# Kernel optimization log

Hardware: AMD Instinct MI355X
Metric: run time of the kernel (lower is better)

The kernel has to match this reference:

```python
import jax, jax.numpy as jnp
import numpy as np

B, L, H, V = 16, 512, 256, 32000
HALF = H // 2
EPS_LN = 1e-5
EPS_NORM = 1e-12


def setup_inputs() -> dict:
    key = jax.random.key(0)
    ks = jax.random.split(key, 9)
    s = 0.02
    return {
        "seq": jax.random.randint(ks[0], (B, L), 0, V),
        "embed": jax.random.normal(ks[1], (V, H), jnp.float32) * s,
        "W1": jax.random.normal(ks[2], (2 * H, H), jnp.float32) * s,
        "b1": jnp.zeros((2 * H,), jnp.float32),
        "W2": jax.random.normal(ks[3], (H, 2 * H), jnp.float32) * s,
        "b2": jnp.zeros((H,), jnp.float32),
        "gamma": jnp.ones((H,), jnp.float32),
        "beta": jnp.zeros((H,), jnp.float32),
        "W_sem": jax.random.normal(ks[4], (HALF, H), jnp.float32) * s,
        "W_epi": jax.random.normal(ks[5], (HALF, H), jnp.float32) * s,
        "W_rp": jax.random.normal(ks[6], (H, H), jnp.float32) * s,
        "b_rp": jnp.zeros((H,), jnp.float32),
        "W_out": jax.random.normal(ks[7], (V, H), jnp.float32) * s,
        "b_out": jnp.zeros((V,), jnp.float32),
    }


def _l2norm(x):
    # F.normalize(dim=-1): x / max(||x||, eps)
    n = jnp.sqrt(jnp.sum(x * x, axis=-1, keepdims=True))
    return x / jnp.maximum(n, EPS_NORM)


def reference(seq, embed, W1, b1, W2, b2, gamma, beta, W_sem, W_epi, W_rp, b_rp, W_out, b_out):
    h = embed[seq]                                   # [B, L, H]
    ff = jnp.maximum(h @ W1.T + b1, 0.0) @ W2.T + b2  # MLP with 2H hidden
    x = h + ff
    mu = jnp.mean(x, axis=-1, keepdims=True)
    var = jnp.var(x, axis=-1, keepdims=True)
    h = (x - mu) / jnp.sqrt(var + EPS_LN) * gamma + beta  # LayerNorm

    ks_all = jnp.einsum('blh,kh->blk', h, W_sem)     # [B, L, HALF]
    ke_all = jnp.einsum('blh,kh->blk', h, W_epi)

    def step(carry, kv):
        M_s, M_e = carry
        k_s, k_e = kv                                 # [B, HALF] each
        kns = _l2norm(k_s)
        kne = _l2norm(k_e)
        vps = jnp.einsum('bij,bj->bi', M_s, kns)      # read from fast weights
        vpe = jnp.einsum('bij,bj->bi', M_e, kne)
        M_s = M_s + jnp.einsum('bi,bj->bij', k_s - vps, kns)  # delta-rule write
        M_e = M_e + jnp.einsum('bi,bj->bij', k_e - vpe, kne)
        return (M_s, M_e), None

    M0 = jnp.zeros((B, HALF, HALF), h.dtype)
    # scan over timesteps 0..L-2 (time-major)
    (M_s, M_e), _ = jax.lax.scan(
        step, (M0, M0),
        (jnp.swapaxes(ks_all[:, :-1], 0, 1), jnp.swapaxes(ke_all[:, :-1], 0, 1)))

    cs = jnp.einsum('bij,bj->bi', M_s, ks_all[:, -1])  # read with last-token query
    ce = jnp.einsum('bij,bj->bi', M_e, ke_all[:, -1])
    c = jnp.concatenate([cs, ce], axis=-1)             # [B, H]
    r = c @ W_rp.T + b_rp
    return r @ W_out.T + b_out                          # [B, V]
```

## Files before the change

kernel.cpp:

```cpp
#include <hip/hip_runtime.h>

#define B_ 16
#define L_ 512
#define H_ 256
#define V_ 32000
#define HALF_ 128

typedef __attribute__((ext_vector_type(8))) short short8;
typedef __attribute__((ext_vector_type(4))) float floatx4;

__device__ __forceinline__ unsigned short f2bf(float x) {
  unsigned int u = __float_as_uint(x);
  unsigned int r = (u + 0x7FFFu + ((u >> 16) & 1u)) >> 16;
  return (unsigned short)r;
}

template <int CTRL>
__device__ __forceinline__ float dpp_xor_add(float x) {
  int y = __builtin_amdgcn_mov_dpp(__float_as_int(x), CTRL, 0xf, 0xf, true);
  return x + __int_as_float(y);
}

__device__ __forceinline__ float redu16(float p) {
  p = dpp_xor_add<0xB1>(p);
  p = dpp_xor_add<0x4E>(p);
  p = dpp_xor_add<0x141>(p);
  p = dpp_xor_add<0x140>(p);
  return p;
}

__device__ __forceinline__ void async_cp16(const float* g, float* l) {
  __builtin_amdgcn_global_load_lds(
      (const __attribute__((address_space(1))) void*)g,
      (__attribute__((address_space(3))) void*)l, 16, 0, 0);
}

__global__ __launch_bounds__(256) void prep_kernel(const int* __restrict__ seq,
                                                   const float* __restrict__ embed,
                                                   float* __restrict__ h,
                                                   unsigned short* __restrict__ hbf,
                                                   const float* __restrict__ W1,
                                                   const float* __restrict__ W2,
                                                   const float* __restrict__ Ws,
                                                   const float* __restrict__ We,
                                                   unsigned short* __restrict__ W1b,
                                                   unsigned short* __restrict__ W2b,
                                                   unsigned short* __restrict__ Wcb) {
  int blk = blockIdx.x;
  int tid = threadIdx.x;
  if (blk < 2048) {
    int token = blk * 4 + (tid >> 6);
    int lane = tid & 63;
    int row = seq[token];
    float4 v = ((const float4*)(embed + (size_t)row * H_))[lane];
    ((float4*)(h + (size_t)token * H_))[lane] = v;
    ushort4 o;
    o.x = f2bf(v.x); o.y = f2bf(v.y); o.z = f2bf(v.z); o.w = f2bf(v.w);
    *(ushort4*)(hbf + (size_t)token * H_ + lane * 4) = o;
  } else {
    int i = (blk - 2048) * 256 + tid;
    if (i < 131072) W1b[i] = f2bf(W1[i]);
    else if (i < 262144) W2b[i - 131072] = f2bf(W2[i - 131072]);
    else if (i < 294912) Wcb[i - 262144] = f2bf(Ws[i - 262144]);
    else Wcb[i - 262144] = f2bf(We[i - 294912]);
  }
}

template <int MT, bool RELU, bool BIAS, bool RES, bool OUT_BF16>
__global__ __launch_bounds__(256) void gemm_mfma(const unsigned short* __restrict__ A,
                                                 const unsigned short* __restrict__ Bw,
                                                 const float* __restrict__ bias,
                                                 const float* __restrict__ Res,
                                                 float* __restrict__ Cf,
                                                 unsigned short* __restrict__ Cb,
                                                 int M, int N, int K) {
  constexpr int FI = MT / 32;
  __shared__ unsigned short As[MT * 40];
  __shared__ unsigned short Bs[128 * 40];
  int tid = threadIdx.x;
  int wave = tid >> 6, lane = tid & 63;
  int wm = (wave >> 1) * (MT / 2), wn = (wave & 1) * 64;
  int quad = lane >> 4, l15 = lane & 15;
  int bm = blockIdx.y * MT, bn = blockIdx.x * 128;
  int sr = tid >> 2, sq = tid & 3;

  floatx4 zero = {0.f, 0.f, 0.f, 0.f};
  floatx4 acc[FI][4];
#pragma unroll
  for (int fi = 0; fi < FI; fi++)
#pragma unroll
    for (int fj = 0; fj < 4; fj++) acc[fi][fj] = zero;

  uint4 av0, av1, bv0, bv1;
  av0 = *(const uint4*)(A + (size_t)(bm + sr) * K + sq * 8);
  if (MT == 128) av1 = *(const uint4*)(A + (size_t)(bm + 64 + sr) * K + sq * 8);
  bv0 = *(const uint4*)(Bw + (size_t)(bn + sr) * K + sq * 8);
  bv1 = *(const uint4*)(Bw + (size_t)(bn + 64 + sr) * K + sq * 8);

  for (int k0 = 0; k0 < K; k0 += 32) {
    __syncthreads();
    *(uint4*)(As + sr * 40 + sq * 8) = av0;
    if (MT == 128) *(uint4*)(As + (64 + sr) * 40 + sq * 8) = av1;
    *(uint4*)(Bs + sr * 40 + sq * 8) = bv0;
    *(uint4*)(Bs + (64 + sr) * 40 + sq * 8) = bv1;
    __syncthreads();
    if (k0 + 32 < K) {
      av0 = *(const uint4*)(A + (size_t)(bm + sr) * K + k0 + 32 + sq * 8);
      if (MT == 128) av1 = *(const uint4*)(A + (size_t)(bm + 64 + sr) * K + k0 + 32 + sq * 8);
      bv0 = *(const uint4*)(Bw + (size_t)(bn + sr) * K + k0 + 32 + sq * 8);
      bv1 = *(const uint4*)(Bw + (size_t)(bn + 64 + sr) * K + k0 + 32 + sq * 8);
    }
    short8 af[FI], bf[4];
#pragma unroll
    for (int f = 0; f < FI; f++) af[f] = *(const short8*)(As + (wm + f * 16 + l15) * 40 + quad * 8);
#pragma unroll
    for (int f = 0; f < 4; f++) bf[f] = *(const short8*)(Bs + (wn + f * 16 + l15) * 40 + quad * 8);
#pragma unroll
    for (int fi = 0; fi < FI; fi++)
#pragma unroll
      for (int fj = 0; fj < 4; fj++)
        acc[fi][fj] = __builtin_amdgcn_mfma_f32_16x16x32_bf16(af[fi], bf[fj], acc[fi][fj], 0, 0, 0);
  }

#pragma unroll
  for (int fi = 0; fi < FI; fi++) {
#pragma unroll
    for (int fj = 0; fj < 4; fj++) {
      int col = bn + wn + fj * 16 + l15;
      float bb = BIAS ? bias[col] : 0.f;
#pragma unroll
      for (int rg = 0; rg < 4; rg++) {
        int row = bm + wm + fi * 16 + quad * 4 + rg;
        float v = acc[fi][fj][rg] + bb;
        if (RES) v += Res[(size_t)row * N + col];
        if (RELU) v = fmaxf(v, 0.f);
        if (OUT_BF16) Cb[(size_t)row * N + col] = f2bf(v);
        else Cf[(size_t)row * N + col] = v;
      }
    }
  }
}

__global__ void ln_kernel(const float* __restrict__ x, const float* __restrict__ gamma,
                          const float* __restrict__ beta, unsigned short* __restrict__ yb) {
  int row = blockIdx.x;
  int lane = threadIdx.x;
  float4 v = ((const float4*)(x + (size_t)row * H_))[lane];
  float s = v.x + v.y + v.z + v.w;
  float sq = v.x * v.x + v.y * v.y + v.z * v.z + v.w * v.w;
#pragma unroll
  for (int off = 32; off >= 1; off >>= 1) {
    s += __shfl_xor(s, off);
    sq += __shfl_xor(sq, off);
  }
  float mu = s * (1.f / H_);
  float var = sq * (1.f / H_) - mu * mu;
  float inv = rsqrtf(var + 1e-5f);
  float4 g = ((const float4*)gamma)[lane];
  float4 b = ((const float4*)beta)[lane];
  ushort4 o;
  o.x = f2bf((v.x - mu) * inv * g.x + b.x);
  o.y = f2bf((v.y - mu) * inv * g.y + b.y);
  o.z = f2bf((v.z - mu) * inv * g.z + b.z);
  o.w = f2bf((v.w - mu) * inv * g.w + b.w);
  *(ushort4*)(yb + (size_t)row * H_ + lane * 4) = o;
}

__global__ __launch_bounds__(256) void kproj_kernel(const unsigned short* __restrict__ hnb,
                                                    const unsigned short* __restrict__ Wcb,
                                                    float* __restrict__ khat,
                                                    float* __restrict__ kT) {
  __shared__ unsigned short As[32 * 40];
  __shared__ unsigned short Bs[256 * 40];
  int tid = threadIdx.x;
  int wave = tid >> 6, lane = tid & 63;
  int wm = (wave >> 1) * 16, wnh = wave & 1, wn = wnh * 128;
  int quad = lane >> 4, l15 = lane & 15;
  int bm = blockIdx.x * 32;

  floatx4 zero = {0.f, 0.f, 0.f, 0.f};
  floatx4 acc[8];
#pragma unroll
  for (int fj = 0; fj < 8; fj++) acc[fj] = zero;

  int sr = tid >> 2, sq = tid & 3;
  uint4 av, bv[4];
  if (tid < 128) av = *(const uint4*)(hnb + (size_t)(bm + sr) * H_ + sq * 8);
#pragma unroll
  for (int q = 0; q < 4; q++) {
    int unit = q * 256 + tid;
    bv[q] = *(const uint4*)(Wcb + (size_t)(unit >> 2) * H_ + (unit & 3) * 8);
  }

  for (int k0 = 0; k0 < 256; k0 += 32) {
    __syncthreads();
    if (tid < 128) *(uint4*)(As + sr * 40 + sq * 8) = av;
#pragma unroll
    for (int q = 0; q < 4; q++) {
      int unit = q * 256 + tid;
      *(uint4*)(Bs + (unit >> 2) * 40 + (unit & 3) * 8) = bv[q];
    }
    __syncthreads();
    if (k0 + 32 < 256) {
      if (tid < 128) av = *(const uint4*)(hnb + (size_t)(bm + sr) * H_ + k0 + 32 + sq * 8);
#pragma unroll
      for (int q = 0; q < 4; q++) {
        int unit = q * 256 + tid;
        bv[q] = *(const uint4*)(Wcb + (size_t)(unit >> 2) * H_ + k0 + 32 + (unit & 3) * 8);
      }
    }
    short8 af = *(const short8*)(As + (wm + l15) * 40 + quad * 8);
    short8 bf[8];
#pragma unroll
    for (int fj = 0; fj < 8; fj++)
      bf[fj] = *(const short8*)(Bs + (wn + fj * 16 + l15) * 40 + quad * 8);
#pragma unroll
    for (int fj = 0; fj < 8; fj++)
      acc[fj] = __builtin_amdgcn_mfma_f32_16x16x32_bf16(af, bf[fj], acc[fj], 0, 0, 0);
  }

  int b = bm >> 9;
  int idxm = b * 2 + wnh;
  int tloc0 = (bm & 511) + wm + quad * 4;
  float inv[4];
#pragma unroll
  for (int rg = 0; rg < 4; rg++) {
    float ssq = 0.f;
#pragma unroll
    for (int fj = 0; fj < 8; fj++) ssq += acc[fj][rg] * acc[fj][rg];
    ssq = redu16(ssq);
    inv[rg] = 1.f / fmaxf(sqrtf(ssq), 1e-12f);
  }
#pragma unroll
  for (int fj = 0; fj < 8; fj++) {
    int ch = fj * 16 + l15;
    int j = ch >> 2, e = ch & 3;
    int pj = (j & 1) ? (16 + (j >> 1)) : (j >> 1);
    int pcol = pj * 4 + e;
#pragma unroll
    for (int rg = 0; rg < 4; rg++)
      khat[((size_t)idxm * L_ + tloc0 + rg) * HALF_ + pcol] = acc[fj][rg] * inv[rg];
    float4 raw = {acc[fj][0], acc[fj][1], acc[fj][2], acc[fj][3]};
    *(float4*)(kT + (size_t)idxm * (HALF_ * L_) + (size_t)ch * L_ + tloc0) = raw;
  }
}

#define STEP(KP, KR)                                                     \
  do {                                                                   \
    float t0_ = m[0] * KP[0] + m[1] * KP[1];                             \
    float t1_ = m[2] * KP[2] + m[3] * KP[3];                             \
    float t2_ = m[4] * KP[4] + m[5] * KP[5];                             \
    float t3_ = m[6] * KP[6] + m[7] * KP[7];                             \
    float p_ = (t0_ + t1_) + (t2_ + t3_);                                \
    p_ = redu16(p_);                                                     \
    float s_ = (KR) - p_;                                                \
    m[0] += s_ * KP[0]; m[1] += s_ * KP[1]; m[2] += s_ * KP[2];          \
    m[3] += s_ * KP[3]; m[4] += s_ * KP[4]; m[5] += s_ * KP[5];          \
    m[6] += s_ * KP[6]; m[7] += s_ * KP[7];                              \
  } while (0)

__global__ __launch_bounds__(256) void scan_kernel(const float* __restrict__ khat,
                                                   const float* __restrict__ kT,
                                                   float* __restrict__ c) {
  __shared__ float sk[2][64 * 128];
  int bid = blockIdx.x;
  int idxm = bid & 31;
  int rg = bid >> 5;
  int b = idxm >> 1, mat = idxm & 1;
  const float* kh = khat + (size_t)idxm * L_ * HALF_;
  const float* kTi = kT + (size_t)idxm * HALF_ * L_;

  int tid = threadIdx.x;
  int wave = tid >> 6, lane = tid & 63;
  int seg = tid & 15, rl = tid >> 4;
  int r = rg * 16 + rl;
  int c0 = seg * 8;
  const float* krow = kTi + (size_t)r * L_;

  float m[8];
#pragma unroll
  for (int g = 0; g < 8; g++) m[g] = 0.f;

  {
    const float* g0 = kh + wave * 2048 + lane * 4;
    float* l0 = &sk[0][wave * 2048];
#pragma unroll
    for (int j = 0; j < 8; j++) async_cp16(g0 + j * 256, l0 + j * 256);
  }
  __syncthreads();

  float4 krn = *(const float4*)(krow);
  const float* lb = &sk[0][0] + seg * 4;

  for (int ch = 0; ch < 7; ch++) {
    {
      const float* gs = kh + (size_t)(ch + 1) * 8192 + wave * 2048 + lane * 4;
      float* ls = &sk[(ch + 1) & 1][wave * 2048];
#pragma unroll
      for (int j = 0; j < 8; j++) async_cp16(gs + j * 256, ls + j * 256);
    }
    const float* base = lb + (ch & 1) * 8192;
    float pk[4][8];
#pragma unroll
    for (int u = 0; u < 4; u++) {
      *(float4*)&pk[u][0] = *(const float4*)(base + u * 128);
      *(float4*)&pk[u][4] = *(const float4*)(base + u * 128 + 64);
    }
    for (int g = 0; g < 15; g++) {
      float4 krc = krn;
      krn = *(const float4*)(krow + ch * 64 + g * 4 + 4);
#pragma unroll
      for (int u = 0; u < 4; u++) {
        STEP(pk[u], ((u == 0) ? krc.x : (u == 1) ? krc.y : (u == 2) ? krc.z : krc.w));
        int tn = g * 4 + u + 4;
        *(float4*)&pk[u][0] = *(const float4*)(base + tn * 128);
        *(float4*)&pk[u][4] = *(const float4*)(base + tn * 128 + 64);
      }
    }
    {
      float4 krc = krn;
      krn = *(const float4*)(krow + ch * 64 + 64);
      STEP(pk[0], krc.x);
      STEP(pk[1], krc.y);
      STEP(pk[2], krc.z);
      STEP(pk[3], krc.w);
    }
    __syncthreads();
  }

  {
    const float* base = lb + 8192;
    float pk[4][8];
#pragma unroll
    for (int u = 0; u < 4; u++) {
      *(float4*)&pk[u][0] = *(const float4*)(base + u * 128);
      *(float4*)&pk[u][4] = *(const float4*)(base + u * 128 + 64);
    }
    for (int g = 0; g < 15; g++) {
      float4 krc = krn;
      krn = *(const float4*)(krow + 448 + g * 4 + 4);
#pragma unroll
      for (int u = 0; u < 4; u++) {
        STEP(pk[u], ((u == 0) ? krc.x : (u == 1) ? krc.y : (u == 2) ? krc.z : krc.w));
        int tn = g * 4 + u + 4;
        *(float4*)&pk[u][0] = *(const float4*)(base + tn * 128);
        *(float4*)&pk[u][4] = *(const float4*)(base + tn * 128 + 64);
      }
    }
    float4 krc = krn;
    STEP(pk[0], krc.x);
    STEP(pk[1], krc.y);
    STEP(pk[2], krc.z);
  }

  float q[8];
#pragma unroll
  for (int j = 0; j < 8; j++) q[j] = kTi[(size_t)(c0 + j) * L_ + 511];
  float t0 = m[0] * q[0] + m[1] * q[1];
  float t1 = m[2] * q[2] + m[3] * q[3];
  float t2 = m[4] * q[4] + m[5] * q[5];
  float t3 = m[6] * q[6] + m[7] * q[7];
  float p = redu16((t0 + t1) + (t2 + t3));
  if (seg == 0) c[(size_t)b * H_ + mat * HALF_ + r] = p;
}

__global__ void rp_kernel(const float* __restrict__ c, const float* __restrict__ Wrp,
                          const float* __restrict__ brp, float* __restrict__ r) {
  int b = blockIdx.x;
  int n = threadIdx.x;
  __shared__ float cs[H_];
  cs[n] = c[(size_t)b * H_ + n];
  __syncthreads();
  const float4* w4 = (const float4*)(Wrp + (size_t)n * H_);
  const float4* c4 = (const float4*)cs;
  float acc = 0.f;
#pragma unroll 8
  for (int k = 0; k < H_ / 4; k++) {
    float4 w = w4[k], cc = c4[k];
    acc += w.x * cc.x + w.y * cc.y + w.z * cc.z + w.w * cc.w;
  }
  r[(size_t)b * H_ + n] = acc + brp[n];
}

__global__ __launch_bounds__(256) void out_kernel(const float* __restrict__ r,
                                                  const float* __restrict__ Wout,
                                                  const float* __restrict__ bout,
                                                  float* __restrict__ out) {
  __shared__ float rs[16 * 272];
  __shared__ float obuf[16 * 68];
  int tid = threadIdx.x;
#pragma unroll
  for (int q = 0; q < 16; q++) {
    int idx = q * 256 + tid;
    int bb = idx >> 8, cc = idx & 255;
    rs[bb * 272 + cc + 4 * (cc >> 6)] = r[idx];
  }
  __syncthreads();
  int row = tid >> 2, part = tid & 3;
  int v = blockIdx.x * 64 + row;
  const float4* w4 = (const float4*)(Wout + (size_t)v * H_ + part * 64);
  float acc[16];
#pragma unroll
  for (int bb = 0; bb < 16; bb++) acc[bb] = 0.f;
#pragma unroll 4
  for (int j = 0; j < 16; j++) {
    float4 w = w4[j];
#pragma unroll
    for (int bb = 0; bb < 16; bb++) {
      float4 rv = *(const float4*)&rs[bb * 272 + part * 68 + j * 4];
      acc[bb] += w.x * rv.x + w.y * rv.y + w.z * rv.z + w.w * rv.w;
    }
  }
  float bo = bout[v];
#pragma unroll
  for (int bb = 0; bb < 16; bb++) {
    acc[bb] = dpp_xor_add<0xB1>(acc[bb]);
    acc[bb] = dpp_xor_add<0x4E>(acc[bb]);
  }
#pragma unroll
  for (int q = 0; q < 4; q++) {
    int bb = part * 4 + q;
    obuf[bb * 68 + row] = acc[bb] + bo;
  }
  __syncthreads();
#pragma unroll
  for (int q = 0; q < 4; q++) {
    int idx = q * 256 + tid;
    int bb = idx >> 6, vl = idx & 63;
    out[(size_t)bb * V_ + blockIdx.x * 64 + vl] = obuf[bb * 68 + vl];
  }
}

extern "C" void kernel_launch(void* const* d_in, const int* in_sizes, int n_in,
                              void* d_out, int out_size, void* d_ws, size_t ws_size,
                              hipStream_t stream) {
  const int* seq = (const int*)d_in[0];
  const float* embed = (const float*)d_in[1];
  const float* W1 = (const float*)d_in[2];
  const float* b1 = (const float*)d_in[3];
  const float* W2 = (const float*)d_in[4];
  const float* b2 = (const float*)d_in[5];
  const float* gamma = (const float*)d_in[6];
  const float* beta = (const float*)d_in[7];
  const float* Wsem = (const float*)d_in[8];
  const float* Wepi = (const float*)d_in[9];
  const float* Wrp = (const float*)d_in[10];
  const float* brp = (const float*)d_in[11];
  const float* Wout = (const float*)d_in[12];
  const float* bout = (const float*)d_in[13];
  float* out = (float*)d_out;

  float* ws = (float*)d_ws;
  float* h = ws;
  float* kT = ws;
  unsigned short* a1b = (unsigned short*)(ws + 2097152);
  float* khat = ws + 2097152;
  unsigned short* hbf = (unsigned short*)(ws + 4194304);
  unsigned short* hnb = (unsigned short*)(ws + 5242880);
  unsigned short* W1b = (unsigned short*)(ws + 6291456);
  unsigned short* W2b = (unsigned short*)(ws + 6356992);
  unsigned short* Wcb = (unsigned short*)(ws + 6422528);
  float* c = ws + 6455296;
  float* r = ws + 6459392;

  prep_kernel<<<3328, 256, 0, stream>>>(seq, embed, h, hbf, W1, W2, Wsem, Wepi, W1b, W2b, Wcb);
  gemm_mfma<128, true, true, false, true><<<dim3(4, 64), 256, 0, stream>>>(
      hbf, W1b, b1, nullptr, nullptr, a1b, 8192, 512, 256);
  gemm_mfma<64, false, true, true, false><<<dim3(2, 128), 256, 0, stream>>>(
      a1b, W2b, b2, h, h, nullptr, 8192, 256, 512);
  ln_kernel<<<8192, 64, 0, stream>>>(h, gamma, beta, hnb);
  kproj_kernel<<<256, 256, 0, stream>>>(hnb, Wcb, khat, kT);
  scan_kernel<<<256, 256, 0, stream>>>(khat, kT, c);
  rp_kernel<<<16, 256, 0, stream>>>(c, Wrp, brp, r);
  out_kernel<<<500, 256, 0, stream>>>(r, Wout, bout, out);
}
```

Baseline: 230.9 us.

## Block the delta-rule scan four timesteps at a time using precomputed key Gram terms

The scan kernel now processes four timesteps per group. Each chunk first computes the pairwise dot products of its normalized keys and stores them in shared memory, so the four reductions against M can be issued independently and corrected with a small triangular solve. This replaces the serial dependency chain of one reduction per step with four independent reductions per group. The raw key rows are also staged into padded shared memory instead of being read from global memory per step. The cost is extra Gram computation, an added barrier per chunk, more shared memory and more registers, and the reassociated arithmetic can change floating-point rounding.

```diff
diff --git a/kernel.cpp b/kernel.cpp
--- a/kernel.cpp
+++ b/kernel.cpp
@@ -33,6 +33,14 @@
   __builtin_amdgcn_global_load_lds(
       (const __attribute__((address_space(1))) void*)g,
       (__attribute__((address_space(3))) void*)l, 16, 0, 0);
+}
+
+__device__ __forceinline__ float dot8(const float* a, const float* b) {
+  float t0 = a[0] * b[0] + a[1] * b[1];
+  float t1 = a[2] * b[2] + a[3] * b[3];
+  float t2 = a[4] * b[4] + a[5] * b[5];
+  float t3 = a[6] * b[6] + a[7] * b[7];
+  return (t0 + t1) + (t2 + t3);
 }
 
 __global__ __launch_bounds__(256) void prep_kernel(const int* __restrict__ seq,
@@ -245,24 +253,45 @@
   }
 }
 
-#define STEP(KP, KR)                                                     \
-  do {                                                                   \
-    float t0_ = m[0] * KP[0] + m[1] * KP[1];                             \
-    float t1_ = m[2] * KP[2] + m[3] * KP[3];                             \
-    float t2_ = m[4] * KP[4] + m[5] * KP[5];                             \
-    float t3_ = m[6] * KP[6] + m[7] * KP[7];                             \
-    float p_ = (t0_ + t1_) + (t2_ + t3_);                                \
-    p_ = redu16(p_);                                                     \
-    float s_ = (KR) - p_;                                                \
-    m[0] += s_ * KP[0]; m[1] += s_ * KP[1]; m[2] += s_ * KP[2];          \
-    m[3] += s_ * KP[3]; m[4] += s_ * KP[4]; m[5] += s_ * KP[5];          \
-    m[6] += s_ * KP[6]; m[7] += s_ * KP[7];                              \
+
+#define LOADPK(P, TL)                                                          \
+  do {                                                                         \
+    _Pragma("unroll") for (int u_ = 0; u_ < 4; u_++) {                         \
+      *(float4*)&P[u_][0] = *(const float4*)(base + ((TL) + u_) * 128);        \
+      *(float4*)&P[u_][4] = *(const float4*)(base + ((TL) + u_) * 128 + 64);   \
+    }                                                                          \
+  } while (0)
+
+#define GRP4(P, PN, TL, DOLOAD)                                                \
+  do {                                                                         \
+    if (DOLOAD) LOADPK(PN, (TL) + 4);                                          \
+    float4 krc_ = *(const float4*)(krp + (TL));                                \
+    float4 aA_ = *(const float4*)&a_s[(TL) >> 2][0];                           \
+    float2 aB_ = *(const float2*)&a_s[(TL) >> 2][4];                           \
+    float P0_ = redu16(dot8(m, P[0]));                                         \
+    float P1_ = redu16(dot8(m, P[1]));                                         \
+    float P2_ = redu16(dot8(m, P[2]));                                         \
+    float P3_ = redu16(dot8(m, P[3]));                                         \
+    float s0_ = krc_.x - P0_;                                                  \
+    float s1_ = (krc_.y - P1_) - s0_ * aA_.x;                                  \
+    float s2_ = (krc_.z - P2_) - (s0_ * aA_.y + s1_ * aA_.z);                  \
+    float s3_ = (krc_.w - P3_) - ((s0_ * aA_.w + s1_ * aB_.x) + s2_ * aB_.y);  \
+    _Pragma("unroll") for (int j_ = 0; j_ < 8; j_++) {                         \
+      float mm_ = m[j_];                                                       \
+      mm_ += s0_ * P[0][j_];                                                   \
+      mm_ += s1_ * P[1][j_];                                                   \
+      mm_ += s2_ * P[2][j_];                                                   \
+      mm_ += s3_ * P[3][j_];                                                   \
+      m[j_] = mm_;                                                             \
+    }                                                                          \
   } while (0)
 
 __global__ __launch_bounds__(256) void scan_kernel(const float* __restrict__ khat,
                                                    const float* __restrict__ kT,
                                                    float* __restrict__ c) {
   __shared__ float sk[2][64 * 128];
+  __shared__ float krs[16 * 520];
+  __shared__ float a_s[16][8];
   int bid = blockIdx.x;
   int idxm = bid & 31;
   int rg = bid >> 5;
@@ -271,96 +300,90 @@
   const float* kTi = kT + (size_t)idxm * HALF_ * L_;
 
   int tid = threadIdx.x;
-  int wave = tid >> 6, lane = tid & 63;
+  int wv = tid >> 6, ln = tid & 63;
   int seg = tid & 15, rl = tid >> 4;
   int r = rg * 16 + rl;
   int c0 = seg * 8;
-  const float* krow = kTi + (size_t)r * L_;
 
   float m[8];
 #pragma unroll
   for (int g = 0; g < 8; g++) m[g] = 0.f;
 
   {
-    const float* g0 = kh + wave * 2048 + lane * 4;
-    float* l0 = &sk[0][wave * 2048];
+    const float* gk = kTi + (size_t)rg * 16 * 512;
+    float4 krv[8];
+#pragma unroll
+    for (int j = 0; j < 8; j++) krv[j] = *(const float4*)(gk + wv * 2048 + j * 256 + ln * 4);
+    const float* g0 = kh + wv * 2048 + ln * 4;
+    float* l0 = &sk[0][wv * 2048];
 #pragma unroll
     for (int j = 0; j < 8; j++) async_cp16(g0 + j * 256, l0 + j * 256);
+#pragma unroll
+    for (int j = 0; j < 8; j++) {
+      int idx = wv * 2048 + j * 256 + ln * 4;
+      *(float4*)(krs + (idx >> 9) * 520 + (idx & 511)) = krv[j];
+    }
   }
   __syncthreads();
 
-  float4 krn = *(const float4*)(krow);
-  const float* lb = &sk[0][0] + seg * 4;
-
-  for (int ch = 0; ch < 7; ch++) {
+  for (int ch = 0; ch < 8; ch++) {
+    if (ch < 7) {
+      const float* gs = kh + (size_t)(ch + 1) * 8192 + wv * 2048 + ln * 4;
+      float* ls = &sk[(ch + 1) & 1][wv * 2048];
+#pragma unroll
+      for (int j = 0; j < 8; j++) async_cp16(gs + j * 256, ls + j * 256);
+    }
+    const float* base = &sk[ch & 1][0] + seg * 4;
     {
-      const float* gs = kh + (size_t)(ch + 1) * 8192 + wave * 2048 + lane * 4;
-      float* ls = &sk[(ch + 1) & 1][wave * 2048];
-#pragma unroll
-      for (int j = 0; j < 8; j++) async_cp16(gs + j * 256, ls + j * 256);
-    }
-    const float* base = lb + (ch & 1) * 8192;
-    float pk[4][8];
-#pragma unroll
-    for (int u = 0; u < 4; u++) {
-      *(float4*)&pk[u][0] = *(const float4*)(base + u * 128);
-      *(float4*)&pk[u][4] = *(const float4*)(base + u * 128 + 64);
-    }
-    for (int g = 0; g < 15; g++) {
-      float4 krc = krn;
-      krn = *(const float4*)(krow + ch * 64 + g * 4 + 4);
+      float kv[4][8];
 #pragma unroll
       for (int u = 0; u < 4; u++) {
-        STEP(pk[u], ((u == 0) ? krc.x : (u == 1) ? krc.y : (u == 2) ? krc.z : krc.w));
-        int tn = g * 4 + u + 4;
-        *(float4*)&pk[u][0] = *(const float4*)(base + tn * 128);
-        *(float4*)&pk[u][4] = *(const float4*)(base + tn * 128 + 64);
+        *(float4*)&kv[u][0] = *(const float4*)(base + (rl * 4 + u) * 128);
+        *(float4*)&kv[u][4] = *(const float4*)(base + (rl * 4 + u) * 128 + 64);
       }
-    }
-    {
-      float4 krc = krn;
-      krn = *(const float4*)(krow + ch * 64 + 64);
-      STEP(pk[0], krc.x);
-      STEP(pk[1], krc.y);
-      STEP(pk[2], krc.z);
-      STEP(pk[3], krc.w);
-    }
-    __syncthreads();
-  }
-
-  {
-    const float* base = lb + 8192;
-    float pk[4][8];
-#pragma unroll
-    for (int u = 0; u < 4; u++) {
-      *(float4*)&pk[u][0] = *(const float4*)(base + u * 128);
-      *(float4*)&pk[u][4] = *(const float4*)(base + u * 128 + 64);
-    }
-    for (int g = 0; g < 15; g++) {
-      float4 krc = krn;
-      krn = *(const float4*)(krow + 448 + g * 4 + 4);
-#pragma unroll
-      for (int u = 0; u < 4; u++) {
-        STEP(pk[u], ((u == 0) ? krc.x : (u == 1) ? krc.y : (u == 2) ? krc.z : krc.w));
-        int tn = g * 4 + u + 4;
-        *(float4*)&pk[u][0] = *(const float4*)(base + tn * 128);
-        *(float4*)&pk[u][4] = *(const float4*)(base + tn * 128 + 64);
+      float d10 = redu16(dot8(kv[1], kv[0]));
+      float d20 = redu16(dot8(kv[2], kv[0]));
+      float d21 = redu16(dot8(kv[2], kv[1]));
+      float d30 = redu16(dot8(kv[3], kv[0]));
+      float d31 = redu16(dot8(kv[3], kv[1]));
+      float d32 = redu16(dot8(kv[3], kv[2]));
+      if (seg == 0) {
+        a_s[rl][0] = d10; a_s[rl][1] = d20; a_s[rl][2] = d21;
+        a_s[rl][3] = d30; a_s[rl][4] = d31; a_s[rl][5] = d32;
       }
     }
-    float4 krc = krn;
-    STEP(pk[0], krc.x);
-    STEP(pk[1], krc.y);
-    STEP(pk[2], krc.z);
+    __syncthreads();
+
+    const float* krp = krs + rl * 520 + ch * 64;
+    float pA[4][8], pB[4][8];
+    LOADPK(pA, 0);
+    for (int g = 0; g < 7; g++) {
+      GRP4(pA, pB, g * 8, 1);
+      GRP4(pB, pA, g * 8 + 4, 1);
+    }
+    GRP4(pA, pB, 56, 1);
+    if (ch < 7) {
+      GRP4(pB, pA, 60, 0);
+    } else {
+      float4 krc = *(const float4*)(krp + 60);
+      float4 aA = *(const float4*)&a_s[15][0];
+      float P0 = redu16(dot8(m, pB[0]));
+      float P1 = redu16(dot8(m, pB[1]));
+      float P2 = redu16(dot8(m, pB[2]));
+      float s0 = krc.x - P0;
+      float s1 = (krc.y - P1) - s0 * aA.x;
+      float s2 = (krc.z - P2) - (s0 * aA.y + s1 * aA.z);
+#pragma unroll
+      for (int j = 0; j < 8; j++)
+        m[j] += s0 * pB[0][j] + s1 * pB[1][j] + s2 * pB[2][j];
+    }
+    __syncthreads();
   }
 
   float q[8];
 #pragma unroll
   for (int j = 0; j < 8; j++) q[j] = kTi[(size_t)(c0 + j) * L_ + 511];
-  float t0 = m[0] * q[0] + m[1] * q[1];
-  float t1 = m[2] * q[2] + m[3] * q[3];
-  float t2 = m[4] * q[4] + m[5] * q[5];
-  float t3 = m[6] * q[6] + m[7] * q[7];
-  float p = redu16((t0 + t1) + (t2 + t3));
+  float p = redu16(dot8(m, q));
   if (seg == 0) c[(size_t)b * H_ + mat * HALF_ + r] = p;
 }
 
```

Measured after the change: 232.3 us. Within noise of the previous version (+0.6%).

## Split scan rows across 32 lanes and double the scan grid

Applied to the files above, without the earlier changes.

The delta-rule scan now gives each matrix row to 32 lanes holding 4 columns each, where before 16 lanes held 8 columns each. This halves the per-thread state and doubles the block count to 512, and the reduction gains a ds_swizzle stage. The khat permuted-column layout and the async global-to-LDS double buffer are replaced by a register-staged prefetch into a single LDS buffer with two barriers per chunk. The per-row key stream is also staged in LDS. The aim is more parallelism on the latency-bound sequential scan, at the cost of a longer reduction chain per step and more synchronisation.

```diff
diff --git a/kernel.cpp b/kernel.cpp
--- a/kernel.cpp
+++ b/kernel.cpp
@@ -29,10 +29,10 @@
   return p;
 }
 
-__device__ __forceinline__ void async_cp16(const float* g, float* l) {
-  __builtin_amdgcn_global_load_lds(
-      (const __attribute__((address_space(1))) void*)g,
-      (__attribute__((address_space(3))) void*)l, 16, 0, 0);
+__device__ __forceinline__ float redu32(float p) {
+  p = redu16(p);
+  int y = __builtin_amdgcn_ds_swizzle(__float_as_int(p), 0x401F);
+  return p + __int_as_float(y);
 }
 
 __global__ __launch_bounds__(256) void prep_kernel(const int* __restrict__ seq,
@@ -234,35 +234,29 @@
 #pragma unroll
   for (int fj = 0; fj < 8; fj++) {
     int ch = fj * 16 + l15;
-    int j = ch >> 2, e = ch & 3;
-    int pj = (j & 1) ? (16 + (j >> 1)) : (j >> 1);
-    int pcol = pj * 4 + e;
 #pragma unroll
     for (int rg = 0; rg < 4; rg++)
-      khat[((size_t)idxm * L_ + tloc0 + rg) * HALF_ + pcol] = acc[fj][rg] * inv[rg];
+      khat[((size_t)idxm * L_ + tloc0 + rg) * HALF_ + ch] = acc[fj][rg] * inv[rg];
     float4 raw = {acc[fj][0], acc[fj][1], acc[fj][2], acc[fj][3]};
     *(float4*)(kT + (size_t)idxm * (HALF_ * L_) + (size_t)ch * L_ + tloc0) = raw;
   }
 }
 
-#define STEP(KP, KR)                                                     \
-  do {                                                                   \
-    float t0_ = m[0] * KP[0] + m[1] * KP[1];                             \
-    float t1_ = m[2] * KP[2] + m[3] * KP[3];                             \
-    float t2_ = m[4] * KP[4] + m[5] * KP[5];                             \
-    float t3_ = m[6] * KP[6] + m[7] * KP[7];                             \
-    float p_ = (t0_ + t1_) + (t2_ + t3_);                                \
-    p_ = redu16(p_);                                                     \
-    float s_ = (KR) - p_;                                                \
-    m[0] += s_ * KP[0]; m[1] += s_ * KP[1]; m[2] += s_ * KP[2];          \
-    m[3] += s_ * KP[3]; m[4] += s_ * KP[4]; m[5] += s_ * KP[5];          \
-    m[6] += s_ * KP[6]; m[7] += s_ * KP[7];                              \
+
+#define STEP(PK, KR)                                     \
+  do {                                                   \
+    float p_ = (m0 * PK.x + m1 * PK.y) + (m2 * PK.z + m3 * PK.w); \
+    p_ = redu32(p_);                                     \
+    float s_ = (KR) - p_;                                \
+    m0 += s_ * PK.x; m1 += s_ * PK.y;                    \
+    m2 += s_ * PK.z; m3 += s_ * PK.w;                    \
   } while (0)
 
 __global__ __launch_bounds__(256) void scan_kernel(const float* __restrict__ khat,
                                                    const float* __restrict__ kT,
                                                    float* __restrict__ c) {
-  __shared__ float sk[2][64 * 128];
+  __shared__ float sk[64 * 128];
+  __shared__ float krs[8 * 512];
   int bid = blockIdx.x;
   int idxm = bid & 31;
   int rg = bid >> 5;
@@ -271,97 +265,71 @@
   const float* kTi = kT + (size_t)idxm * HALF_ * L_;
 
   int tid = threadIdx.x;
-  int wave = tid >> 6, lane = tid & 63;
-  int seg = tid & 15, rl = tid >> 4;
-  int r = rg * 16 + rl;
-  int c0 = seg * 8;
-  const float* krow = kTi + (size_t)r * L_;
-
-  float m[8];
-#pragma unroll
-  for (int g = 0; g < 8; g++) m[g] = 0.f;
-
+  int rl = tid >> 5;
+  int l32 = tid & 31;
+  int r = rg * 8 + rl;
+  int c0 = l32 * 4;
+
+  float m0 = 0.f, m1 = 0.f, m2 = 0.f, m3 = 0.f;
+
+  float4 krv[4], nxt[8];
   {
-    const float* g0 = kh + wave * 2048 + lane * 4;
-    float* l0 = &sk[0][wave * 2048];
-#pragma unroll
-    for (int j = 0; j < 8; j++) async_cp16(g0 + j * 256, l0 + j * 256);
+    const float* gk = kTi + (size_t)rg * 8 * L_;
+#pragma unroll
+    for (int j = 0; j < 4; j++) krv[j] = *(const float4*)(gk + (j * 256 + tid) * 4);
+#pragma unroll
+    for (int j = 0; j < 8; j++) nxt[j] = *(const float4*)(kh + (j * 256 + tid) * 4);
+#pragma unroll
+    for (int j = 0; j < 4; j++) *(float4*)(krs + (j * 256 + tid) * 4) = krv[j];
+#pragma unroll
+    for (int j = 0; j < 8; j++) *(float4*)(sk + (j * 256 + tid) * 4) = nxt[j];
   }
   __syncthreads();
 
-  float4 krn = *(const float4*)(krow);
-  const float* lb = &sk[0][0] + seg * 4;
-
-  for (int ch = 0; ch < 7; ch++) {
-    {
-      const float* gs = kh + (size_t)(ch + 1) * 8192 + wave * 2048 + lane * 4;
-      float* ls = &sk[(ch + 1) & 1][wave * 2048];
-#pragma unroll
-      for (int j = 0; j < 8; j++) async_cp16(gs + j * 256, ls + j * 256);
-    }
-    const float* base = lb + (ch & 1) * 8192;
-    float pk[4][8];
-#pragma unroll
-    for (int u = 0; u < 4; u++) {
-      *(float4*)&pk[u][0] = *(const float4*)(base + u * 128);
-      *(float4*)&pk[u][4] = *(const float4*)(base + u * 128 + 64);
-    }
+  const float* krp = krs + rl * 512;
+  const float* base = sk + c0;
+
+  for (int ch = 0; ch < 8; ch++) {
+    if (ch < 7) {
+#pragma unroll
+      for (int j = 0; j < 8; j++)
+        nxt[j] = *(const float4*)(kh + (size_t)(ch + 1) * 8192 + (j * 256 + tid) * 4);
+    }
+    const float* krq = krp + ch * 64;
+    float4 pk0 = *(const float4*)(base + 0 * 128);
+    float4 pk1 = *(const float4*)(base + 1 * 128);
+    float4 pk2 = *(const float4*)(base + 2 * 128);
+    float4 pk3 = *(const float4*)(base + 3 * 128);
+    float4 krn = *(const float4*)(krq);
     for (int g = 0; g < 15; g++) {
       float4 krc = krn;
-      krn = *(const float4*)(krow + ch * 64 + g * 4 + 4);
-#pragma unroll
-      for (int u = 0; u < 4; u++) {
-        STEP(pk[u], ((u == 0) ? krc.x : (u == 1) ? krc.y : (u == 2) ? krc.z : krc.w));
-        int tn = g * 4 + u + 4;
-        *(float4*)&pk[u][0] = *(const float4*)(base + tn * 128);
-        *(float4*)&pk[u][4] = *(const float4*)(base + tn * 128 + 64);
-      }
+      krn = *(const float4*)(krq + g * 4 + 4);
+      STEP(pk0, krc.x); pk0 = *(const float4*)(base + (g * 4 + 4) * 128);
+      STEP(pk1, krc.y); pk1 = *(const float4*)(base + (g * 4 + 5) * 128);
+      STEP(pk2, krc.z); pk2 = *(const float4*)(base + (g * 4 + 6) * 128);
+      STEP(pk3, krc.w); pk3 = *(const float4*)(base + (g * 4 + 7) * 128);
     }
     {
       float4 krc = krn;
-      krn = *(const float4*)(krow + ch * 64 + 64);
-      STEP(pk[0], krc.x);
-      STEP(pk[1], krc.y);
-      STEP(pk[2], krc.z);
-      STEP(pk[3], krc.w);
-    }
-    __syncthreads();
-  }
-
-  {
-    const float* base = lb + 8192;
-    float pk[4][8];
-#pragma unroll
-    for (int u = 0; u < 4; u++) {
-      *(float4*)&pk[u][0] = *(const float4*)(base + u * 128);
-      *(float4*)&pk[u][4] = *(const float4*)(base + u * 128 + 64);
-    }
-    for (int g = 0; g < 15; g++) {
-      float4 krc = krn;
-      krn = *(const float4*)(krow + 448 + g * 4 + 4);
-#pragma unroll
-      for (int u = 0; u < 4; u++) {
-        STEP(pk[u], ((u == 0) ? krc.x : (u == 1) ? krc.y : (u == 2) ? krc.z : krc.w));
-        int tn = g * 4 + u + 4;
-        *(float4*)&pk[u][0] = *(const float4*)(base + tn * 128);
-        *(float4*)&pk[u][4] = *(const float4*)(base + tn * 128 + 64);
-      }
-    }
-    float4 krc = krn;
-    STEP(pk[0], krc.x);
-    STEP(pk[1], krc.y);
-    STEP(pk[2], krc.z);
-  }
-
-  float q[8];
-#pragma unroll
-  for (int j = 0; j < 8; j++) q[j] = kTi[(size_t)(c0 + j) * L_ + 511];
-  float t0 = m[0] * q[0] + m[1] * q[1];
-  float t1 = m[2] * q[2] + m[3] * q[3];
-  float t2 = m[4] * q[4] + m[5] * q[5];
-  float t3 = m[6] * q[6] + m[7] * q[7];
-  float p = redu16((t0 + t1) + (t2 + t3));
-  if (seg == 0) c[(size_t)b * H_ + mat * HALF_ + r] = p;
+      STEP(pk0, krc.x);
+      STEP(pk1, krc.y);
+      STEP(pk2, krc.z);
+      if (ch < 7) STEP(pk3, krc.w);
+    }
+    __syncthreads();
+    if (ch < 7) {
+#pragma unroll
+      for (int j = 0; j < 8; j++) *(float4*)(sk + (j * 256 + tid) * 4) = nxt[j];
+    }
+    __syncthreads();
+  }
+
+  float q0 = kTi[(size_t)(c0 + 0) * L_ + 511];
+  float q1 = kTi[(size_t)(c0 + 1) * L_ + 511];
+  float q2 = kTi[(size_t)(c0 + 2) * L_ + 511];
+  float q3 = kTi[(size_t)(c0 + 3) * L_ + 511];
+  float p = redu32((m0 * q0 + m1 * q1) + (m2 * q2 + m3 * q3));
+  if (l32 == 0) c[(size_t)b * H_ + mat * HALF_ + r] = p;
 }
 
 __global__ void rp_kernel(const float* __restrict__ c, const float* __restrict__ Wrp,
@@ -470,7 +438,7 @@
       a1b, W2b, b2, h, h, nullptr, 8192, 256, 512);
   ln_kernel<<<8192, 64, 0, stream>>>(h, gamma, beta, hnb);
   kproj_kernel<<<256, 256, 0, stream>>>(hnb, Wcb, khat, kT);
-  scan_kernel<<<256, 256, 0, stream>>>(khat, kT, c);
+  scan_kernel<<<512, 256, 0, stream>>>(khat, kT, c);
   rp_kernel<<<16, 256, 0, stream>>>(c, Wrp, brp, r);
   out_kernel<<<500, 256, 0, stream>>>(r, Wout, bout, out);
 }
```

New measurement: 261.8 us. +13.4%, slower.
